# Kernel optimization log

Hardware: AMD Instinct MI355X
Metric: run time of the kernel (lower is better)

The kernel has to match this reference:

```python
import jax, jax.numpy as jnp
import numpy as np

B, S, H, NH = 2, 2048, 4096, 32
HD = H // NH
BETA = 1.0
INV_NORM = 1.0 / float(np.sqrt(HD))


def setup_inputs() -> dict:
    key = jax.random.key(0)
    ks = jax.random.split(key, 8)
    return {
        "hidden_states": jax.random.normal(ks[0], (B, S, H), jnp.float32),
        "residual": jax.random.normal(ks[1], (B, S, H), jnp.float32),
        "alibi": jax.random.normal(ks[2], (B * NH, 1, S), jnp.float32),
        "attention_mask": jax.random.randint(ks[3], (B, 1, S, S), 0, 2).astype(bool),
        "qkv_w": jax.random.normal(ks[4], (3 * H, H), jnp.float32) * 0.02,
        "qkv_b": jax.random.normal(ks[5], (3 * H,), jnp.float32) * 0.02,
        "dense_w": jax.random.normal(ks[6], (H, H), jnp.float32) * 0.02,
        "dense_b": jax.random.normal(ks[7], (H,), jnp.float32) * 0.02,
    }


def reference(hidden_states, residual, alibi, attention_mask, qkv_w, qkv_b, dense_w, dense_b):
    b, s, h = hidden_states.shape
    # fused QKV projection: [b, s, 3h] viewed as [b, s, nh, 3, hd] (BLOOM layout)
    fused = hidden_states @ qkv_w.T + qkv_b
    fused = fused.reshape(b, s, NH, 3, HD)
    q = fused[..., 0, :]  # [b, s, nh, hd]
    k = fused[..., 1, :]
    v = fused[..., 2, :]
    q = q.transpose(0, 2, 1, 3).reshape(b * NH, s, HD)   # [b*nh, s, hd]
    kT = k.transpose(0, 2, 3, 1).reshape(b * NH, HD, s)  # [b*nh, hd, s]
    v = v.transpose(0, 2, 1, 3).reshape(b * NH, s, HD)
    # baddbmm: beta*alibi + alpha * q @ k^T
    scores = BETA * alibi + INV_NORM * jnp.matmul(q, kT)  # [b*nh, s, s]
    scores = scores.reshape(b, NH, s, s)
    neg = jnp.finfo(scores.dtype).min
    scores = jnp.where(attention_mask, neg, scores)
    probs = jax.nn.softmax(scores, axis=-1)
    ctx = jnp.matmul(probs.reshape(b * NH, s, s), v)  # [b*nh, s, hd]
    ctx = ctx.reshape(b, NH, s, HD).transpose(0, 2, 1, 3).reshape(b, s, h)
    out = ctx @ dense_w.T + dense_b + residual  # dropout p applied with training=False => identity
    return out
```

## Files before the change

### kernel.cpp

```cpp
#include <hip/hip_runtime.h>
#include <hip/hip_bf16.h>

#define S_LEN 2048
#define NHEAD 32
#define HDIM  128
#define HSZ   4096
#define NH_TOT 64
#define INV_NORM 0.08838834764831845f
#define NEG_MIN  -3.4028234663852886e38f
#define LOG2E    1.4426950408889634f

typedef __attribute__((ext_vector_type(8))) __bf16 bf16x8;
typedef __attribute__((ext_vector_type(4))) float  floatx4;

__device__ __forceinline__ void gload16(const void* g, void* l) {
  __builtin_amdgcn_global_load_lds(
      (__attribute__((address_space(1))) void*)g,
      (__attribute__((address_space(3))) void*)l, 16, 0, 0);
}

__global__ __launch_bounds__(256) void cvt_f32_bf16(
    const float* __restrict__ in, __hip_bfloat16* __restrict__ out, size_t n)
{
  const size_t i = ((size_t)blockIdx.x * 256 + threadIdx.x) * 4;
  if (i < n) {
    const float4 v = *(const float4*)(in + i);
    __hip_bfloat16 o0 = __float2bfloat16(v.x);
    __hip_bfloat16 o1 = __float2bfloat16(v.y);
    __hip_bfloat16 o2 = __float2bfloat16(v.z);
    __hip_bfloat16 o3 = __float2bfloat16(v.w);
    ushort4 pk;
    pk.x = *(unsigned short*)&o0; pk.y = *(unsigned short*)&o1;
    pk.z = *(unsigned short*)&o2; pk.w = *(unsigned short*)&o3;
    *(ushort4*)(out + i) = pk;
  }
}

__global__ __launch_bounds__(256) void pack_mask(
    const int* __restrict__ mk, unsigned long long* __restrict__ mp)
{
  const size_t gid = (size_t)blockIdx.x * 256 + threadIdx.x;
  const unsigned long long b = __ballot(mk[gid] != 0);
  if ((threadIdx.x & 63) == 0) mp[gid >> 6] = b;
}


#define VM4 asm volatile("s_waitcnt vmcnt(4)" ::: "memory")
#define VM2 asm volatile("s_waitcnt vmcnt(2)" ::: "memory")
#define VM0 asm volatile("s_waitcnt vmcnt(0)" ::: "memory")

#define PHASE(qi, qj, LOADA, STAGE, TAILVM)                                     \
  {                                                                             \
    if (LOADA) {                                                                \
      _Pragma("unroll")                                                         \
      for (int ii = 0; ii < 4; ++ii) {                                          \
        af[ii][0] = *(const bf16x8*)(lds + pb * 16384 +                         \
                     (((qi) * 4 + ii) * 32 + arow) * 64 + ((quad) ^ axor) * 8); \
        af[ii][1] = *(const bf16x8*)(lds + pb * 16384 +                         \
                     (((qi) * 4 + ii) * 32 + arow) * 64 + ((4 + quad) ^ axor) * 8); \
      }                                                                         \
    }                                                                           \
    bf16x8 bq[2][2];                                                            \
    _Pragma("unroll")                                                           \
    for (int jj = 0; jj < 2; ++jj) {                                            \
      bq[jj][0] = *(const bf16x8*)(lds + 32768 + pb * 16384 +                   \
                   (((qj) * 2 + jj) * 64 + brow) * 64 + ((quad) ^ axor) * 8);   \
      bq[jj][1] = *(const bf16x8*)(lds + 32768 + pb * 16384 +                   \
                   (((qj) * 2 + jj) * 64 + brow) * 64 + ((4 + quad) ^ axor) * 8); \
    }                                                                           \
    STAGE;                                                                      \
    __builtin_amdgcn_s_barrier();                                               \
    asm volatile("s_waitcnt lgkmcnt(0)" ::: "memory");                          \
    __builtin_amdgcn_sched_barrier(0);                                          \
    __builtin_amdgcn_s_setprio(1);                                              \
    _Pragma("unroll")                                                           \
    for (int ii = 0; ii < 4; ++ii)                                              \
      _Pragma("unroll")                                                         \
      for (int jj = 0; jj < 2; ++jj) {                                          \
        acc[(qi) * 4 + ii][(qj) * 2 + jj] =                                     \
            __builtin_amdgcn_mfma_f32_16x16x32_bf16(                            \
                af[ii][0], bq[jj][0], acc[(qi) * 4 + ii][(qj) * 2 + jj], 0, 0, 0); \
        acc[(qi) * 4 + ii][(qj) * 2 + jj] =                                     \
            __builtin_amdgcn_mfma_f32_16x16x32_bf16(                            \
                af[ii][1], bq[jj][1], acc[(qi) * 4 + ii][(qj) * 2 + jj], 0, 0, 0); \
      }                                                                         \
    __builtin_amdgcn_s_setprio(0);                                              \
    TAILVM;                                                                     \
    __builtin_amdgcn_s_barrier();                                               \
  }

__global__ __launch_bounds__(512, 2) void qkv_gemm(
    const __hip_bfloat16* __restrict__ A,
    const __hip_bfloat16* __restrict__ W,
    const float* __restrict__ bias,
    __hip_bfloat16* __restrict__ Qb,
    __hip_bfloat16* __restrict__ Kb,
    __hip_bfloat16* __restrict__ Vt)
{
  __shared__ __align__(16) __hip_bfloat16 lds[65536];

  const int wg  = blockIdx.x;
  const int swz = (wg & 7) * 96 + (wg >> 3);
  const int bx  = swz % 48, by = swz / 48;
  const int m0 = by * 256, n0 = bx * 256;

  const int t = threadIdx.x;
  const int w = t >> 6, l = t & 63;
  const int wm = w >> 2, wn = w & 3;
  const int quad = l >> 4, ln = l & 15;
  const int axor = ln & 7;
  const int arow = wm * 16 + ln;
  const int brow = wn * 16 + ln;
  const int srow8 = l >> 3;
  const int sch   = (l & 7) ^ srow8;
  char* ldsB = (char*)lds;

  floatx4 acc[8][4] = {};
  bf16x8 af[4][2];

#define STG_A(pbn, h, ktn)                                                      \
  { _Pragma("unroll")                                                           \
    for (int c = 0; c < 2; ++c)                                                 \
      gload16(A + (size_t)(m0 + (h) * 128 + (c * 8 + w) * 8 + srow8) * 4096 +   \
                  (ktn) * 64 + sch * 8,                                         \
              ldsB + (pbn) * 32768 + (h) * 16384 + (c * 8 + w) * 1024);         \
    __builtin_amdgcn_sched_barrier(0); }
#define STG_B(pbn, h, ktn)                                                      \
  { _Pragma("unroll")                                                           \
    for (int c = 0; c < 2; ++c)                                                 \
      gload16(W + (size_t)(n0 + (h) * 128 + (c * 8 + w) * 8 + srow8) * 4096 +   \
                  (ktn) * 64 + sch * 8,                                         \
              ldsB + 65536 + (pbn) * 32768 + (h) * 16384 + (c * 8 + w) * 1024); \
    __builtin_amdgcn_sched_barrier(0); }

  STG_A(0, 0, 0); STG_B(0, 0, 0); STG_B(0, 1, 0); STG_A(0, 1, 0);
  VM4;
  __builtin_amdgcn_s_barrier();

  int pb = 0;
  for (int kt = 0; kt < 64; ++kt, pb ^= 1) {
    const int ktn = kt + 1;
    const int pbn = pb ^ 1;
    if (ktn < 64) {
      PHASE(0, 0, 1, STG_A(pbn, 0, ktn), VM4)
      PHASE(0, 1, 0, STG_B(pbn, 0, ktn), VM4)
      PHASE(1, 0, 1, STG_B(pbn, 1, ktn), )
      PHASE(1, 1, 0, STG_A(pbn, 1, ktn), VM4)
    } else {
      PHASE(0, 0, 1, , VM2)
      PHASE(0, 1, 0, , VM0)
      PHASE(1, 0, 1, , )
      PHASE(1, 1, 0, , )
    }
  }
#undef STG_A
#undef STG_B

#pragma unroll
  for (int i = 0; i < 8; ++i) {
#pragma unroll
    for (int j = 0; j < 4; ++j) {
      const int n     = n0 + j * 64 + wn * 16 + ln;
      const int nh    = n / 384;
      const int which = (n >> 7) % 3;
      const int hd    = n & 127;
      const float bv  = bias[n];
#pragma unroll
      for (int r = 0; r < 4; ++r) {
        const int m  = m0 + i * 32 + wm * 16 + quad * 4 + r;
        const int bb = m >> 11;
        const int s  = m & 2047;
        const int head = bb * NHEAD + nh;
        const __hip_bfloat16 hv = __float2bfloat16(acc[i][j][r] + bv);
        if (which == 0)      Qb[((size_t)head * S_LEN + s) * HDIM + hd] = hv;
        else if (which == 1) Kb[((size_t)head * S_LEN + s) * HDIM + hd] = hv;
        else                 Vt[((size_t)head * HDIM + hd) * S_LEN + s] = hv;
      }
    }
  }
}

__global__ __launch_bounds__(512, 2) void dense_gemm(
    const __hip_bfloat16* __restrict__ CtxQ,
    const __hip_bfloat16* __restrict__ W,
    const float* __restrict__ bias,
    const float* __restrict__ residual,
    float* __restrict__ out)
{
  __shared__ __align__(16) __hip_bfloat16 lds[65536];

  const int wg  = blockIdx.x;
  const int swz = (wg & 7) * 32 + (wg >> 3);
  const int bx  = swz & 15, by = swz >> 4;
  const int m0 = by * 256, n0 = bx * 256;

  const int t = threadIdx.x;
  const int w = t >> 6, l = t & 63;
  const int wm = w >> 2, wn = w & 3;
  const int quad = l >> 4, ln = l & 15;
  const int axor = ln & 7;
  const int arow = wm * 16 + ln;
  const int brow = wn * 16 + ln;
  const int srow8 = l >> 3;
  const int sch   = (l & 7) ^ srow8;
  char* ldsB = (char*)lds;

  floatx4 acc[8][4] = {};
  bf16x8 af[4][2];

#define STG_A(pbn, h, ktn)                                                      \
  { const int nh_ = (ktn) >> 1;                                                 \
    const int hd_ = ((ktn) & 1) * 64 + sch * 8;                                 \
    _Pragma("unroll")                                                           \
    for (int c = 0; c < 2; ++c) {                                               \
      const int m_ = m0 + (h) * 128 + (c * 8 + w) * 8 + srow8;                  \
      gload16(CtxQ + ((size_t)(((m_ >> 11) * NHEAD + nh_) * S_LEN + (m_ & 2047))) * HDIM + hd_, \
              ldsB + (pbn) * 32768 + (h) * 16384 + (c * 8 + w) * 1024); }       \
    __builtin_amdgcn_sched_barrier(0); }
#define STG_B(pbn, h, ktn)                                                      \
  { _Pragma("unroll")                                                           \
    for (int c = 0; c < 2; ++c)                                                 \
      gload16(W + (size_t)(n0 + (h) * 128 + (c * 8 + w) * 8 + srow8) * 4096 +   \
                  (ktn) * 64 + sch * 8,                                         \
              ldsB + 65536 + (pbn) * 32768 + (h) * 16384 + (c * 8 + w) * 1024); \
    __builtin_amdgcn_sched_barrier(0); }

  STG_A(0, 0, 0); STG_B(0, 0, 0); STG_B(0, 1, 0); STG_A(0, 1, 0);
  VM4;
  __builtin_amdgcn_s_barrier();

  int pb = 0;
  for (int kt = 0; kt < 64; ++kt, pb ^= 1) {
    const int ktn = kt + 1;
    const int pbn = pb ^ 1;
    if (ktn < 64) {
      PHASE(0, 0, 1, STG_A(pbn, 0, ktn), VM4)
      PHASE(0, 1, 0, STG_B(pbn, 0, ktn), VM4)
      PHASE(1, 0, 1, STG_B(pbn, 1, ktn), )
      PHASE(1, 1, 0, STG_A(pbn, 1, ktn), VM4)
    } else {
      PHASE(0, 0, 1, , VM2)
      PHASE(0, 1, 0, , VM0)
      PHASE(1, 0, 1, , )
      PHASE(1, 1, 0, , )
    }
  }
#undef STG_A
#undef STG_B

#pragma unroll
  for (int i = 0; i < 8; ++i) {
#pragma unroll
    for (int j = 0; j < 4; ++j) {
      const int n = n0 + j * 64 + wn * 16 + ln;
      const float bv = bias[n];
#pragma unroll
      for (int r = 0; r < 4; ++r) {
        const int m = m0 + i * 32 + wm * 16 + quad * 4 + r;
        out[(size_t)m * HSZ + n] =
            acc[i][j][r] + bv + residual[(size_t)m * HSZ + n];
      }
    }
  }
}

__global__ __launch_bounds__(256) void flash_attn(
    __hip_bfloat16* __restrict__ Qb,
    const __hip_bfloat16* __restrict__ Kb,
    const __hip_bfloat16* __restrict__ Vt,
    const float* __restrict__ alibi,
    const unsigned long long* __restrict__ mpack)
{
  __shared__ __align__(16) __hip_bfloat16 KsS[2][64 * 128];
  __shared__ __align__(16) __hip_bfloat16 VsS[2][128 * 64];
  __shared__ __align__(16) __hip_bfloat16 Psh[4][16 * 72];

  const int head = blockIdx.x >> 5;
  const int qblk = blockIdx.x & 31;
  const int t = threadIdx.x;
  const int w = t >> 6, l = t & 63;
  const int quad = l >> 4, ln = l & 15;
  const int b = head >> 5;
  const int q0 = qblk * 64 + w * 16;

  __hip_bfloat16* Qh = Qb + (size_t)head * S_LEN * HDIM;
  const __hip_bfloat16* Kh = Kb + (size_t)head * S_LEN * HDIM;
  const __hip_bfloat16* Vh = Vt + (size_t)head * HDIM * S_LEN;
  const float* al = alibi + (size_t)head * S_LEN;
  const unsigned long long* mkp = mpack + (size_t)b * S_LEN * (S_LEN / 64);

#define STAGE_KV(kj, Ks, Vs)                                                   \
  {                                                                            \
    _Pragma("unroll")                                                          \
    for (int c = 0; c < 4; ++c) {                                              \
      const int s   = (w * 4 + c) * 64 + l;                                    \
      const int row = s >> 4, ch = s & 15;                                     \
      const int g   = ch ^ (row & 7);                                          \
      gload16(Kh + (size_t)((kj) + row) * HDIM + g * 8,                        \
              (char*)(Ks) + (w * 4 + c) * 1024);                               \
    }                                                                          \
    _Pragma("unroll")                                                          \
    for (int c = 0; c < 4; ++c) {                                              \
      const int s   = (w * 4 + c) * 64 + l;                                    \
      const int row = s >> 3, ch = s & 7;                                      \
      const int g   = ch ^ (row & 7);                                          \
      gload16(Vh + (size_t)row * S_LEN + (kj) + g * 8,                         \
              (char*)(Vs) + (w * 4 + c) * 1024);                               \
    }                                                                          \
  }

  STAGE_KV(0, KsS[0], VsS[0]);

  bf16x8 qf[4];
#pragma unroll
  for (int ks = 0; ks < 4; ++ks)
    qf[ks] = *(const bf16x8*)(Qh + (size_t)(q0 + ln) * HDIM + ks * 32 + quad * 8);

  float m_run[4], lpart[4], alp[4], sv[4][4];
  floatx4 accO[8] = {};
#pragma unroll
  for (int r = 0; r < 4; ++r) { m_run[r] = -INFINITY; lpart[r] = 0.f; }

  __hip_bfloat16* Pw = Psh[w];
  const float SC = INV_NORM * LOG2E;
  const int ln7 = ln & 7;

  __syncthreads();

  for (int kj0 = 0, it = 0; kj0 < S_LEN; kj0 += 64, ++it) {
    const int cur = it & 1;
    const __hip_bfloat16* Kc = KsS[cur];
    const __hip_bfloat16* Vc = VsS[cur];

    if (kj0 + 64 < S_LEN) STAGE_KV(kj0 + 64, KsS[cur ^ 1], VsS[cur ^ 1]);

    unsigned long long mb[4];
#pragma unroll
    for (int r = 0; r < 4; ++r)
      mb[r] = mkp[(size_t)(q0 + quad * 4 + r) * (S_LEN / 64) + (kj0 >> 6)];
    float av[4];
#pragma unroll
    for (int tt = 0; tt < 4; ++tt)
      av[tt] = al[kj0 + tt * 16 + ln] * LOG2E;

#pragma unroll
    for (int tt = 0; tt < 4; ++tt) {
      floatx4 accS = {};
#pragma unroll
      for (int ks = 0; ks < 4; ++ks) {
        const int row = tt * 16 + ln;
        const int c   = (ks * 4 + quad) ^ ln7;
        bf16x8 kf = *(const bf16x8*)(Kc + row * 128 + c * 8);
        accS = __builtin_amdgcn_mfma_f32_16x16x32_bf16(qf[ks], kf, accS, 0, 0, 0);
      }
#pragma unroll
      for (int r = 0; r < 4; ++r) {
        float s = accS[r] * SC + av[tt];
        if ((mb[r] >> (tt * 16 + ln)) & 1ull) s = NEG_MIN;
        sv[tt][r] = s;
      }
    }

    bool resc = false;
#pragma unroll
    for (int r = 0; r < 4; ++r) {
      float cm = fmaxf(fmaxf(sv[0][r], sv[1][r]), fmaxf(sv[2][r], sv[3][r]));
      cm = fmaxf(cm, __shfl_xor(cm, 1, 64));
      cm = fmaxf(cm, __shfl_xor(cm, 2, 64));
      cm = fmaxf(cm, __shfl_xor(cm, 4, 64));
      cm = fmaxf(cm, __shfl_xor(cm, 8, 64));
      const float mn = fmaxf(m_run[r], cm);
      const float a  = __builtin_amdgcn_exp2f(m_run[r] - mn);
      alp[r] = a;
      if (a != 1.f) resc = true;
      m_run[r] = mn;
      float ps = 0.f;
#pragma unroll
      for (int tt = 0; tt < 4; ++tt) {
        const float p = __builtin_amdgcn_exp2f(sv[tt][r] - mn);
        sv[tt][r] = p;
        ps += p;
      }
      lpart[r] = lpart[r] * a + ps;
    }
    if (__any(resc)) {
#pragma unroll
      for (int dt = 0; dt < 8; ++dt)
#pragma unroll
        for (int r = 0; r < 4; ++r) accO[dt][r] *= alp[r];
    }

#pragma unroll
    for (int tt = 0; tt < 4; ++tt)
#pragma unroll
      for (int r = 0; r < 4; ++r)
        Pw[(quad * 4 + r) * 72 + tt * 16 + ln] = __float2bfloat16(sv[tt][r]);
    __builtin_amdgcn_wave_barrier();
    const bf16x8 pf0 = *(const bf16x8*)(Pw + ln * 72 + quad * 8);
    const bf16x8 pf1 = *(const bf16x8*)(Pw + ln * 72 + 32 + quad * 8);

#pragma unroll
    for (int dt = 0; dt < 8; ++dt) {
      const int row = dt * 16 + ln;
      const int c0  = quad ^ ln7;
      const int c1  = (4 + quad) ^ ln7;
      bf16x8 vf0 = *(const bf16x8*)(Vc + row * 64 + c0 * 8);
      bf16x8 vf1 = *(const bf16x8*)(Vc + row * 64 + c1 * 8);
      accO[dt] = __builtin_amdgcn_mfma_f32_16x16x32_bf16(pf0, vf0, accO[dt], 0, 0, 0);
      accO[dt] = __builtin_amdgcn_mfma_f32_16x16x32_bf16(pf1, vf1, accO[dt], 0, 0, 0);
    }
    __builtin_amdgcn_wave_barrier();

    __syncthreads();
  }
#undef STAGE_KV

#pragma unroll
  for (int r = 0; r < 4; ++r) {
    float ps = lpart[r];
    ps += __shfl_xor(ps, 1, 64);
    ps += __shfl_xor(ps, 2, 64);
    ps += __shfl_xor(ps, 4, 64);
    ps += __shfl_xor(ps, 8, 64);
    const int qi = q0 + quad * 4 + r;
    const float invl = 1.0f / ps;
#pragma unroll
    for (int dt = 0; dt < 8; ++dt)
      Qh[(size_t)qi * HDIM + dt * 16 + ln] = __float2bfloat16(accO[dt][r] * invl);
  }
}

extern "C" void kernel_launch(void* const* d_in, const int* in_sizes, int n_in,
                              void* d_out, int out_size, void* d_ws, size_t ws_size,
                              hipStream_t stream) {
  const float* hidden   = (const float*)d_in[0];
  const float* residual = (const float*)d_in[1];
  const float* alibi    = (const float*)d_in[2];
  const int*   mask     = (const int*)d_in[3];
  const float* qkv_w    = (const float*)d_in[4];
  const float* qkv_b    = (const float*)d_in[5];
  const float* dense_w  = (const float*)d_in[6];
  const float* dense_b  = (const float*)d_in[7];
  float* out = (float*)d_out;

  const size_t per  = (size_t)NH_TOT * S_LEN * HDIM;
  const size_t nWq  = (size_t)3 * HSZ * HSZ;
  __hip_bfloat16* Qb = (__hip_bfloat16*)d_ws;
  __hip_bfloat16* Kb = Qb + per;
  __hip_bfloat16* Vt = Kb + per;
  __hip_bfloat16* Ah = Vt + per;
  __hip_bfloat16* Wq = Ah + per;
  unsigned long long* mp = (unsigned long long*)Wq;

  cvt_f32_bf16<<<(int)(per / 4 / 256), 256, 0, stream>>>(hidden, Ah, per);
  cvt_f32_bf16<<<(int)(nWq / 4 / 256), 256, 0, stream>>>(qkv_w, Wq, nWq);

  qkv_gemm<<<dim3(768), 512, 0, stream>>>(Ah, Wq, qkv_b, Qb, Kb, Vt);

  pack_mask<<<(int)(2u * S_LEN * S_LEN / 256), 256, 0, stream>>>(mask, mp);
  cvt_f32_bf16<<<(int)(per / 4 / 256), 256, 0, stream>>>(dense_w, Ah, per);

  flash_attn<<<dim3(2048), 256, 0, stream>>>(Qb, Kb, Vt, alibi, mp);
  dense_gemm<<<dim3(256), 512, 0, stream>>>(Qb, Ah, dense_b, residual, out);
}
```

Before: 1.288 ms.

## Process two query tiles per wave in flash attention to reuse K/V fragments

Each wave now handles 32 query rows (two 16-row groups) instead of 16, so the block covers 128 queries and the grid halves to 1024 blocks. Every K and V fragment read from LDS now feeds two MFMAs, which halves LDS traffic and K/V global staging per query. V is no longer double-buffered: it is loaded into a single buffer at the start of each iteration, and an extra block-wide barrier separates the P writes from the PV stage. This raises register pressure (launch bounds ask for 2 blocks per CU) and exposes V load latency within each iteration.

```diff
diff --git a/kernel.cpp b/kernel.cpp
--- a/kernel.cpp
+++ b/kernel.cpp
@@ -264,7 +264,7 @@
   }
 }
 
-__global__ __launch_bounds__(256) void flash_attn(
+__global__ __launch_bounds__(256, 2) void flash_attn(
     __hip_bfloat16* __restrict__ Qb,
     const __hip_bfloat16* __restrict__ Kb,
     const __hip_bfloat16* __restrict__ Vt,
@@ -272,16 +272,16 @@
     const unsigned long long* __restrict__ mpack)
 {
   __shared__ __align__(16) __hip_bfloat16 KsS[2][64 * 128];
-  __shared__ __align__(16) __hip_bfloat16 VsS[2][128 * 64];
-  __shared__ __align__(16) __hip_bfloat16 Psh[4][16 * 72];
-
-  const int head = blockIdx.x >> 5;
-  const int qblk = blockIdx.x & 31;
+  __shared__ __align__(16) __hip_bfloat16 Vs[128 * 64];
+  __shared__ __align__(16) __hip_bfloat16 Psh[4][2][16 * 72];
+
+  const int head = blockIdx.x >> 4;
+  const int qblk = blockIdx.x & 15;
   const int t = threadIdx.x;
   const int w = t >> 6, l = t & 63;
   const int quad = l >> 4, ln = l & 15;
   const int b = head >> 5;
-  const int q0 = qblk * 64 + w * 16;
+  const int q0 = qblk * 128 + w * 32;
 
   __hip_bfloat16* Qh = Qb + (size_t)head * S_LEN * HDIM;
   const __hip_bfloat16* Kh = Kb + (size_t)head * S_LEN * HDIM;
@@ -289,39 +289,41 @@
   const float* al = alibi + (size_t)head * S_LEN;
   const unsigned long long* mkp = mpack + (size_t)b * S_LEN * (S_LEN / 64);
 
-#define STAGE_KV(kj, Ks, Vs)                                                   \
-  {                                                                            \
-    _Pragma("unroll")                                                          \
+#define STAGE_K(kj, Ks)                                                        \
+  { _Pragma("unroll")                                                          \
     for (int c = 0; c < 4; ++c) {                                              \
       const int s   = (w * 4 + c) * 64 + l;                                    \
       const int row = s >> 4, ch = s & 15;                                     \
       const int g   = ch ^ (row & 7);                                          \
       gload16(Kh + (size_t)((kj) + row) * HDIM + g * 8,                        \
               (char*)(Ks) + (w * 4 + c) * 1024);                               \
-    }                                                                          \
-    _Pragma("unroll")                                                          \
+    } }
+#define STAGE_V(kj)                                                            \
+  { _Pragma("unroll")                                                          \
     for (int c = 0; c < 4; ++c) {                                              \
       const int s   = (w * 4 + c) * 64 + l;                                    \
       const int row = s >> 3, ch = s & 7;                                      \
       const int g   = ch ^ (row & 7);                                          \
       gload16(Vh + (size_t)row * S_LEN + (kj) + g * 8,                         \
               (char*)(Vs) + (w * 4 + c) * 1024);                               \
-    }                                                                          \
-  }
-
-  STAGE_KV(0, KsS[0], VsS[0]);
-
-  bf16x8 qf[4];
-#pragma unroll
-  for (int ks = 0; ks < 4; ++ks)
-    qf[ks] = *(const bf16x8*)(Qh + (size_t)(q0 + ln) * HDIM + ks * 32 + quad * 8);
-
-  float m_run[4], lpart[4], alp[4], sv[4][4];
-  floatx4 accO[8] = {};
-#pragma unroll
-  for (int r = 0; r < 4; ++r) { m_run[r] = -INFINITY; lpart[r] = 0.f; }
-
-  __hip_bfloat16* Pw = Psh[w];
+    } }
+
+  STAGE_K(0, KsS[0]);
+
+  bf16x8 qf[2][4];
+#pragma unroll
+  for (int g = 0; g < 2; ++g)
+#pragma unroll
+    for (int ks = 0; ks < 4; ++ks)
+      qf[g][ks] = *(const bf16x8*)(Qh + (size_t)(q0 + g * 16 + ln) * HDIM + ks * 32 + quad * 8);
+
+  float m_run[2][4], lpart[2][4], alp[2][4], sv[2][4][4];
+  floatx4 accO[2][8] = {};
+#pragma unroll
+  for (int g = 0; g < 2; ++g)
+#pragma unroll
+    for (int r = 0; r < 4; ++r) { m_run[g][r] = -INFINITY; lpart[g][r] = 0.f; }
+
   const float SC = INV_NORM * LOG2E;
   const int ln7 = ln & 7;
 
@@ -330,14 +332,16 @@
   for (int kj0 = 0, it = 0; kj0 < S_LEN; kj0 += 64, ++it) {
     const int cur = it & 1;
     const __hip_bfloat16* Kc = KsS[cur];
-    const __hip_bfloat16* Vc = VsS[cur];
-
-    if (kj0 + 64 < S_LEN) STAGE_KV(kj0 + 64, KsS[cur ^ 1], VsS[cur ^ 1]);
-
-    unsigned long long mb[4];
-#pragma unroll
-    for (int r = 0; r < 4; ++r)
-      mb[r] = mkp[(size_t)(q0 + quad * 4 + r) * (S_LEN / 64) + (kj0 >> 6)];
+
+    STAGE_V(kj0);
+    if (kj0 + 64 < S_LEN) STAGE_K(kj0 + 64, KsS[cur ^ 1]);
+
+    unsigned long long mb[2][4];
+#pragma unroll
+    for (int g = 0; g < 2; ++g)
+#pragma unroll
+      for (int r = 0; r < 4; ++r)
+        mb[g][r] = mkp[(size_t)(q0 + g * 16 + quad * 4 + r) * (S_LEN / 64) + (kj0 >> 6)];
     float av[4];
 #pragma unroll
     for (int tt = 0; tt < 4; ++tt)
@@ -345,88 +349,108 @@
 
 #pragma unroll
     for (int tt = 0; tt < 4; ++tt) {
-      floatx4 accS = {};
+      floatx4 accS0 = {}, accS1 = {};
 #pragma unroll
       for (int ks = 0; ks < 4; ++ks) {
         const int row = tt * 16 + ln;
         const int c   = (ks * 4 + quad) ^ ln7;
         bf16x8 kf = *(const bf16x8*)(Kc + row * 128 + c * 8);
-        accS = __builtin_amdgcn_mfma_f32_16x16x32_bf16(qf[ks], kf, accS, 0, 0, 0);
+        accS0 = __builtin_amdgcn_mfma_f32_16x16x32_bf16(qf[0][ks], kf, accS0, 0, 0, 0);
+        accS1 = __builtin_amdgcn_mfma_f32_16x16x32_bf16(qf[1][ks], kf, accS1, 0, 0, 0);
       }
 #pragma unroll
       for (int r = 0; r < 4; ++r) {
-        float s = accS[r] * SC + av[tt];
-        if ((mb[r] >> (tt * 16 + ln)) & 1ull) s = NEG_MIN;
-        sv[tt][r] = s;
+        float s0 = accS0[r] * SC + av[tt];
+        float s1 = accS1[r] * SC + av[tt];
+        if ((mb[0][r] >> (tt * 16 + ln)) & 1ull) s0 = NEG_MIN;
+        if ((mb[1][r] >> (tt * 16 + ln)) & 1ull) s1 = NEG_MIN;
+        sv[0][tt][r] = s0;
+        sv[1][tt][r] = s1;
       }
     }
 
     bool resc = false;
 #pragma unroll
+    for (int g = 0; g < 2; ++g)
+#pragma unroll
     for (int r = 0; r < 4; ++r) {
-      float cm = fmaxf(fmaxf(sv[0][r], sv[1][r]), fmaxf(sv[2][r], sv[3][r]));
+      float cm = fmaxf(fmaxf(sv[g][0][r], sv[g][1][r]), fmaxf(sv[g][2][r], sv[g][3][r]));
       cm = fmaxf(cm, __shfl_xor(cm, 1, 64));
       cm = fmaxf(cm, __shfl_xor(cm, 2, 64));
       cm = fmaxf(cm, __shfl_xor(cm, 4, 64));
       cm = fmaxf(cm, __shfl_xor(cm, 8, 64));
-      const float mn = fmaxf(m_run[r], cm);
-      const float a  = __builtin_amdgcn_exp2f(m_run[r] - mn);
-      alp[r] = a;
+      const float mn = fmaxf(m_run[g][r], cm);
+      const float a  = __builtin_amdgcn_exp2f(m_run[g][r] - mn);
+      alp[g][r] = a;
       if (a != 1.f) resc = true;
-      m_run[r] = mn;
+      m_run[g][r] = mn;
       float ps = 0.f;
 #pragma unroll
       for (int tt = 0; tt < 4; ++tt) {
-        const float p = __builtin_amdgcn_exp2f(sv[tt][r] - mn);
-        sv[tt][r] = p;
+        const float p = __builtin_amdgcn_exp2f(sv[g][tt][r] - mn);
+        sv[g][tt][r] = p;
         ps += p;
       }
-      lpart[r] = lpart[r] * a + ps;
+      lpart[g][r] = lpart[g][r] * a + ps;
     }
     if (__any(resc)) {
 #pragma unroll
-      for (int dt = 0; dt < 8; ++dt)
-#pragma unroll
-        for (int r = 0; r < 4; ++r) accO[dt][r] *= alp[r];
-    }
-
-#pragma unroll
-    for (int tt = 0; tt < 4; ++tt)
-#pragma unroll
-      for (int r = 0; r < 4; ++r)
-        Pw[(quad * 4 + r) * 72 + tt * 16 + ln] = __float2bfloat16(sv[tt][r]);
-    __builtin_amdgcn_wave_barrier();
-    const bf16x8 pf0 = *(const bf16x8*)(Pw + ln * 72 + quad * 8);
-    const bf16x8 pf1 = *(const bf16x8*)(Pw + ln * 72 + 32 + quad * 8);
+      for (int g = 0; g < 2; ++g)
+#pragma unroll
+        for (int dt = 0; dt < 8; ++dt)
+#pragma unroll
+          for (int r = 0; r < 4; ++r) accO[g][dt][r] *= alp[g][r];
+    }
+
+#pragma unroll
+    for (int g = 0; g < 2; ++g)
+#pragma unroll
+      for (int tt = 0; tt < 4; ++tt)
+#pragma unroll
+        for (int r = 0; r < 4; ++r)
+          Psh[w][g][(quad * 4 + r) * 72 + tt * 16 + ln] = __float2bfloat16(sv[g][tt][r]);
+
+    __syncthreads();
+
+    bf16x8 pfr[2][2];
+#pragma unroll
+    for (int g = 0; g < 2; ++g) {
+      pfr[g][0] = *(const bf16x8*)(&Psh[w][g][0] + ln * 72 + quad * 8);
+      pfr[g][1] = *(const bf16x8*)(&Psh[w][g][0] + ln * 72 + 32 + quad * 8);
+    }
 
 #pragma unroll
     for (int dt = 0; dt < 8; ++dt) {
       const int row = dt * 16 + ln;
       const int c0  = quad ^ ln7;
       const int c1  = (4 + quad) ^ ln7;
-      bf16x8 vf0 = *(const bf16x8*)(Vc + row * 64 + c0 * 8);
-      bf16x8 vf1 = *(const bf16x8*)(Vc + row * 64 + c1 * 8);
-      accO[dt] = __builtin_amdgcn_mfma_f32_16x16x32_bf16(pf0, vf0, accO[dt], 0, 0, 0);
-      accO[dt] = __builtin_amdgcn_mfma_f32_16x16x32_bf16(pf1, vf1, accO[dt], 0, 0, 0);
-    }
-    __builtin_amdgcn_wave_barrier();
+      bf16x8 vf0 = *(const bf16x8*)(Vs + row * 64 + c0 * 8);
+      bf16x8 vf1 = *(const bf16x8*)(Vs + row * 64 + c1 * 8);
+      accO[0][dt] = __builtin_amdgcn_mfma_f32_16x16x32_bf16(pfr[0][0], vf0, accO[0][dt], 0, 0, 0);
+      accO[0][dt] = __builtin_amdgcn_mfma_f32_16x16x32_bf16(pfr[0][1], vf1, accO[0][dt], 0, 0, 0);
+      accO[1][dt] = __builtin_amdgcn_mfma_f32_16x16x32_bf16(pfr[1][0], vf0, accO[1][dt], 0, 0, 0);
+      accO[1][dt] = __builtin_amdgcn_mfma_f32_16x16x32_bf16(pfr[1][1], vf1, accO[1][dt], 0, 0, 0);
+    }
 
     __syncthreads();
   }
-#undef STAGE_KV
-
+#undef STAGE_K
+#undef STAGE_V
+
+#pragma unroll
+  for (int g = 0; g < 2; ++g)
 #pragma unroll
   for (int r = 0; r < 4; ++r) {
-    float ps = lpart[r];
+    float ps = lpart[g][r];
     ps += __shfl_xor(ps, 1, 64);
     ps += __shfl_xor(ps, 2, 64);
     ps += __shfl_xor(ps, 4, 64);
     ps += __shfl_xor(ps, 8, 64);
-    const int qi = q0 + quad * 4 + r;
+    const int qi = q0 + g * 16 + quad * 4 + r;
     const float invl = 1.0f / ps;
 #pragma unroll
     for (int dt = 0; dt < 8; ++dt)
-      Qh[(size_t)qi * HDIM + dt * 16 + ln] = __float2bfloat16(accO[dt][r] * invl);
+      Qh[(size_t)qi * HDIM + dt * 16 + ln] = __float2bfloat16(accO[g][dt][r] * invl);
   }
 }
 
@@ -460,6 +484,6 @@
   pack_mask<<<(int)(2u * S_LEN * S_LEN / 256), 256, 0, stream>>>(mask, mp);
   cvt_f32_bf16<<<(int)(per / 4 / 256), 256, 0, stream>>>(dense_w, Ah, per);
 
-  flash_attn<<<dim3(2048), 256, 0, stream>>>(Qb, Kb, Vt, alibi, mp);
+  flash_attn<<<dim3(1024), 256, 0, stream>>>(Qb, Kb, Vt, alibi, mp);
   dense_gemm<<<dim3(256), 512, 0, stream>>>(Qb, Ah, dense_b, residual, out);
 }
```

After: 1.184 ms. 1.09x faster.
